# Kernel optimization log

Measured on AMD Instinct MI355X. Metric: run time of the kernel, lower is better.

## Reference

```python
import jax, jax.numpy as jnp
import numpy as np

SUBSTEPS = 4  # fixed dopri5 substeps per output interval
S0, I0, R0 = 0.99, 0.01, 0.0


def _dopri5_step(f, y, dt):
    # Classic Dormand-Prince 5(4) tableau; 5th-order solution needs stages 1,3,4,5,6.
    k1 = f(y)
    k2 = f(y + dt * (1.0 / 5.0) * k1)
    k3 = f(y + dt * (3.0 / 40.0 * k1 + 9.0 / 40.0 * k2))
    k4 = f(y + dt * (44.0 / 45.0 * k1 - 56.0 / 15.0 * k2 + 32.0 / 9.0 * k3))
    k5 = f(y + dt * (19372.0 / 6561.0 * k1 - 25360.0 / 2187.0 * k2
                     + 64448.0 / 6561.0 * k3 - 212.0 / 729.0 * k4))
    k6 = f(y + dt * (9017.0 / 3168.0 * k1 - 355.0 / 33.0 * k2
                     + 46732.0 / 5247.0 * k3 + 49.0 / 176.0 * k4
                     - 5103.0 / 18656.0 * k5))
    return y + dt * (35.0 / 384.0 * k1 + 500.0 / 1113.0 * k3
                     + 125.0 / 192.0 * k4 - 2187.0 / 6784.0 * k5
                     + 11.0 / 84.0 * k6)


def _solve_sir(beta, gamma, t):
    def f(y):
        S, I, R = y[0], y[1], y[2]
        dS = -beta * S * I
        dI = beta * S * I - gamma * I
        dR = gamma * I
        return jnp.stack([dS, dI, dR])

    y0 = jnp.array([S0, I0, R0], dtype=jnp.float32)
    dts = jnp.diff(t)  # [T-1]

    def interval(y, dt):
        h = dt / SUBSTEPS
        def sub(y, _):
            return _dopri5_step(f, y, h), None
        y, _ = jax.lax.scan(sub, y, None, length=SUBSTEPS)
        return y, y

    _, ys = jax.lax.scan(interval, y0, dts)
    return jnp.concatenate([y0[None, :], ys], axis=0)  # [T, 3]


def setup_inputs() -> dict:
    key = jax.random.key(0)
    ks = jax.random.split(key, 14)
    D_IN, D_OUT, T = 8192, 8192, 8192
    s = 0.02
    inp = {
        "x": jax.random.normal(ks[0], (1, D_IN), dtype=jnp.float32),
        "t": jnp.arange(T, dtype=jnp.float32) * (10.0 / T),
        # Encoder: D_IN -> 128 -> 64 -> 2
        "enc_w1": jax.random.normal(ks[1], (D_IN, 128), dtype=jnp.float32) * s,
        "enc_b1": jnp.zeros((128,), dtype=jnp.float32),
        "enc_w2": jax.random.normal(ks[2], (128, 64), dtype=jnp.float32) * s,
        "enc_b2": jnp.zeros((64,), dtype=jnp.float32),
        "enc_w3": jax.random.normal(ks[3], (64, 2), dtype=jnp.float32) * s,
        "enc_b3": jnp.zeros((2,), dtype=jnp.float32),
        # Decoder: 3 -> 64 -> 128 -> D_OUT
        "dec_w1": jax.random.normal(ks[4], (3, 64), dtype=jnp.float32) * s,
        "dec_b1": jnp.zeros((64,), dtype=jnp.float32),
        "dec_w2": jax.random.normal(ks[5], (64, 128), dtype=jnp.float32) * s,
        "dec_b2": jnp.zeros((128,), dtype=jnp.float32),
        "dec_w3": jax.random.normal(ks[6], (128, D_OUT), dtype=jnp.float32) * s,
        "dec_b3": jnp.zeros((D_OUT,), dtype=jnp.float32),
    }
    return inp


def reference(x, t, enc_w1, enc_b1, enc_w2, enc_b2, enc_w3, enc_b3,
              dec_w1, dec_b1, dec_w2, dec_b2, dec_w3, dec_b3):
    # Encoder (batch=1, matching the original's scalar-unbind SIR semantics)
    h = jax.nn.relu(x @ enc_w1 + enc_b1)
    h = jax.nn.relu(h @ enc_w2 + enc_b2)
    p = h @ enc_w3 + enc_b3            # [1, 2]
    beta, gamma = p[0, 0], p[0, 1]

    sol = _solve_sir(beta, gamma, t)   # [T, 3]

    # Decoder
    h = jax.nn.relu(sol @ dec_w1 + dec_b1)
    h = jax.nn.relu(h @ dec_w2 + dec_b2)
    out = jax.nn.relu(h @ dec_w3 + dec_b3)  # [T, D_OUT]
    return out
```

## Files before the change

### kernel.cpp

```cpp
#include <hip/hip_runtime.h>
#include <math.h>
#include <stdint.h>


typedef __attribute__((ext_vector_type(8))) short short8_t;
typedef __attribute__((ext_vector_type(4))) float f32x4;

#define DT_C 0.001220703125f

__device__ __forceinline__ unsigned short f2bf_rn(float f) {
  unsigned int u = __float_as_uint(f);
  unsigned int r = (u + 0x7fffu + ((u >> 16) & 1u)) >> 16;
  return (unsigned short)r;
}
__device__ __forceinline__ float bf2f(unsigned short h) {
  return __uint_as_float(((unsigned int)h) << 16);
}

__device__ __forceinline__ void gl2lds16(const void* g, void* lds_base) {
  __builtin_amdgcn_global_load_lds(
      (const __attribute__((address_space(1))) unsigned int*)(uintptr_t)g,
      (__attribute__((address_space(3))) unsigned int*)(uintptr_t)lds_base,
      16, 0, 0);
}


__device__ __forceinline__ void f_sir(float beta, float gamma,
                                      const float y[3], float d[3]) {
  float SI = y[0] * y[1];
  d[0] = -beta * SI;
  d[1] = beta * SI - gamma * y[1];
  d[2] = gamma * y[1];
}

__device__ __forceinline__ void dopri5_step(float beta, float gamma,
                                            float y[3], float dt) {
  float k1[3], k2[3], k3[3], k4[3], k5[3], k6[3], tmp[3];
  f_sir(beta, gamma, y, k1);
#pragma unroll
  for (int c = 0; c < 3; ++c)
    tmp[c] = y[c] + dt * (0.2f * k1[c]);
  f_sir(beta, gamma, tmp, k2);
#pragma unroll
  for (int c = 0; c < 3; ++c)
    tmp[c] = y[c] + dt * (0.075f * k1[c] + 0.225f * k2[c]);
  f_sir(beta, gamma, tmp, k3);
#pragma unroll
  for (int c = 0; c < 3; ++c)
    tmp[c] = y[c] + dt * ((44.0f / 45.0f) * k1[c] + (-56.0f / 15.0f) * k2[c] +
                          (32.0f / 9.0f) * k3[c]);
  f_sir(beta, gamma, tmp, k4);
#pragma unroll
  for (int c = 0; c < 3; ++c)
    tmp[c] = y[c] + dt * ((19372.0f / 6561.0f) * k1[c] +
                          (-25360.0f / 2187.0f) * k2[c] +
                          (64448.0f / 6561.0f) * k3[c] +
                          (-212.0f / 729.0f) * k4[c]);
  f_sir(beta, gamma, tmp, k5);
#pragma unroll
  for (int c = 0; c < 3; ++c)
    tmp[c] = y[c] + dt * ((9017.0f / 3168.0f) * k1[c] +
                          (-355.0f / 33.0f) * k2[c] +
                          (46732.0f / 5247.0f) * k3[c] +
                          (49.0f / 176.0f) * k4[c] +
                          (-5103.0f / 18656.0f) * k5[c]);
  f_sir(beta, gamma, tmp, k6);
#pragma unroll
  for (int c = 0; c < 3; ++c)
    y[c] = y[c] + dt * ((35.0f / 384.0f) * k1[c] +
                        (500.0f / 1113.0f) * k3[c] +
                        (125.0f / 192.0f) * k4[c] +
                        (-2187.0f / 6784.0f) * k5[c] +
                        (11.0f / 84.0f) * k6[c]);
}

__global__ __launch_bounds__(256) void enc1_kernel(
    const float* __restrict__ x, const float* __restrict__ w1,
    float* __restrict__ partial) {
  __shared__ float4 sh[256];
  int tid = threadIdx.x;
  int j4 = tid & 31, kh = tid >> 5;
  int kbase = blockIdx.x * 128 + kh * 16;
  float4 a; a.x = 0.f; a.y = 0.f; a.z = 0.f; a.w = 0.f;
#pragma unroll
  for (int r = 0; r < 16; ++r) {
    int k = kbase + r;
    float xv = x[k];
    float4 wv = *(const float4*)(w1 + (size_t)k * 128 + j4 * 4);
    a.x = fmaf(xv, wv.x, a.x);
    a.y = fmaf(xv, wv.y, a.y);
    a.z = fmaf(xv, wv.z, a.z);
    a.w = fmaf(xv, wv.w, a.w);
  }
  sh[tid] = a;
  __syncthreads();
  if (tid < 32) {
    float4 s = sh[tid];
#pragma unroll
    for (int h = 1; h < 8; ++h) {
      float4 o = sh[h * 32 + tid];
      s.x += o.x; s.y += o.y; s.z += o.z; s.w += o.w;
    }
    *(float4*)(partial + blockIdx.x * 128 + tid * 4) = s;
  }
}

__global__ __launch_bounds__(256) void prep_kernel(
    const float* __restrict__ partial, const float* __restrict__ b1,
    const float* __restrict__ w2, const float* __restrict__ b2,
    const float* __restrict__ w3, const float* __restrict__ b3,
    float* __restrict__ bg, float* __restrict__ ys) {
  __shared__ float h1s[128];
  __shared__ float h2s[64];
  __shared__ float bgs[2];
  __shared__ float Y0[16][3];
  __shared__ float Y1[256][3];
  int t = threadIdx.x;
  if (t < 128) {
    float s = b1[t];
    for (int b = 0; b < 64; ++b) s += partial[b * 128 + t];
    h1s[t] = fmaxf(s, 0.0f);
  }
  __syncthreads();
  if (t < 64) {
    float a = b2[t];
    for (int k = 0; k < 128; ++k) a = fmaf(h1s[k], w2[k * 64 + t], a);
    h2s[t] = fmaxf(a, 0.0f);
  }
  __syncthreads();
  if (t < 2) {
    float p = b3[t];
    for (int k = 0; k < 64; ++k) p = fmaf(h2s[k], w3[k * 2 + t], p);
    bgs[t] = p;
    bg[t] = p;
  }
  __syncthreads();
  float beta = bgs[0], gamma = bgs[1];
  if (t == 0) {
    float y[3] = {0.99f, 0.01f, 0.0f};
    Y0[0][0] = y[0]; Y0[0][1] = y[1]; Y0[0][2] = y[2];
    for (int j = 1; j < 16; ++j) {
      dopri5_step(beta, gamma, y, 512.0f * DT_C);
      Y0[j][0] = y[0]; Y0[j][1] = y[1]; Y0[j][2] = y[2];
    }
  }
  __syncthreads();
  if (t < 16) {
    float y[3] = {Y0[t][0], Y0[t][1], Y0[t][2]};
    Y1[t * 16][0] = y[0]; Y1[t * 16][1] = y[1]; Y1[t * 16][2] = y[2];
    for (int s = 1; s < 16; ++s) {
      dopri5_step(beta, gamma, y, 32.0f * DT_C);
      Y1[t * 16 + s][0] = y[0]; Y1[t * 16 + s][1] = y[1]; Y1[t * 16 + s][2] = y[2];
    }
  }
  __syncthreads();
  {
    float y[3] = {Y1[t][0], Y1[t][1], Y1[t][2]};
    ys[(t * 8) * 3 + 0] = y[0]; ys[(t * 8) * 3 + 1] = y[1]; ys[(t * 8) * 3 + 2] = y[2];
    for (int s = 1; s < 8; ++s) {
      dopri5_step(beta, gamma, y, 4.0f * DT_C);
      ys[(t * 8 + s) * 3 + 0] = y[0];
      ys[(t * 8 + s) * 3 + 1] = y[1];
      ys[(t * 8 + s) * 3 + 2] = y[2];
    }
  }
}

__global__ __launch_bounds__(256) void wprep_kernel(
    const float* __restrict__ w3, unsigned short* __restrict__ Wt) {
  __shared__ float tl[128 * 65];
  int tid = threadIdx.x;
  int n0 = blockIdx.x * 64;
#pragma unroll
  for (int e = 0; e < 32; ++e) {
    int idx = e * 256 + tid;
    int k = idx >> 6, c = idx & 63;
    tl[k * 65 + c] = w3[(size_t)k * 8192 + n0 + c];
  }
  __syncthreads();
  int nl = tid >> 2, q = tid & 3;
#pragma unroll
  for (int w = 0; w < 4; ++w) {
    int k0 = q * 32 + w * 8;
    short8_t vh, vl;
#pragma unroll
    for (int jj = 0; jj < 8; ++jj) {
      float v = tl[(k0 + jj) * 65 + nl];
      unsigned short h = f2bf_rn(v);
      vh[jj] = (short)h;
      vl[jj] = (short)f2bf_rn(v - bf2f(h));
    }
    *(short8_t*)(Wt + (size_t)(n0 + nl) * 256 + k0) = vh;
    *(short8_t*)(Wt + (size_t)(n0 + nl) * 256 + 128 + k0) = vl;
  }
}

__global__ __launch_bounds__(256) void dec12f_kernel(
    const float* __restrict__ bg, const float* __restrict__ ys,
    const float* __restrict__ w1, const float* __restrict__ b1,
    const float* __restrict__ w2, const float* __restrict__ b2,
    unsigned short* __restrict__ Apack) {
  __shared__ float sols[128 * 4];
  __shared__ float w1s[192];
  __shared__ float b1s[64];
  __shared__ float b2s[128];
  __shared__ float h1s[128 * 66];
  int tid = threadIdx.x;
  int i0 = blockIdx.x * 128;
  if (tid < 192) w1s[tid] = w1[tid];
  if (tid < 64) b1s[tid] = b1[tid];
  if (tid < 128) b2s[tid] = b2[tid];
  if (tid < 33) {
    const float h = 0.25f * DT_C;
    float beta = bg[0], gamma = bg[1];
    int w = blockIdx.x * 32 + tid - 1;
    if (w < 0) {
      sols[0] = 0.99f; sols[1] = 0.01f; sols[2] = 0.0f;
    } else {
      float y[3] = {ys[w * 3 + 0], ys[w * 3 + 1], ys[w * 3 + 2]};
#pragma unroll
      for (int iv = 0; iv < 4; ++iv) {
        dopri5_step(beta, gamma, y, h);
        dopri5_step(beta, gamma, y, h);
        dopri5_step(beta, gamma, y, h);
        dopri5_step(beta, gamma, y, h);
        int local = 4 * w + iv + 1 - i0;
        if (local >= 0 && local < 128) {
          sols[local * 4 + 0] = y[0];
          sols[local * 4 + 1] = y[1];
          sols[local * 4 + 2] = y[2];
        }
      }
    }
  }
  __syncthreads();
#pragma unroll
  for (int e = 0; e < 32; ++e) {
    int idx = e * 256 + tid;
    int i = idx >> 6, j = idx & 63;
    float v = b1s[j];
    v = fmaf(sols[i * 4 + 0], w1s[j], v);
    v = fmaf(sols[i * 4 + 1], w1s[64 + j], v);
    v = fmaf(sols[i * 4 + 2], w1s[128 + j], v);
    h1s[i * 66 + j] = fmaxf(v, 0.0f);
  }
  __syncthreads();
  int tx = tid & 15, ty = tid >> 4;
  float acc[8][8];
#pragma unroll
  for (int a = 0; a < 8; ++a)
#pragma unroll
    for (int b = 0; b < 8; ++b) acc[a][b] = 0.0f;
  for (int j = 0; j < 64; ++j) {
    float a[8];
#pragma unroll
    for (int mm = 0; mm < 8; ++mm) a[mm] = h1s[(ty * 8 + mm) * 66 + j];
    float4 q0 = *(const float4*)(w2 + j * 128 + tx * 8);
    float4 q1 = *(const float4*)(w2 + j * 128 + tx * 8 + 4);
    float b[8] = {q0.x, q0.y, q0.z, q0.w, q1.x, q1.y, q1.z, q1.w};
#pragma unroll
    for (int mm = 0; mm < 8; ++mm)
#pragma unroll
      for (int nn = 0; nn < 8; ++nn)
        acc[mm][nn] = fmaf(a[mm], b[nn], acc[mm][nn]);
  }
#pragma unroll
  for (int mm = 0; mm < 8; ++mm) {
    int row = i0 + ty * 8 + mm;
    short8_t vh, vl;
#pragma unroll
    for (int nn = 0; nn < 8; ++nn) {
      float v = fmaxf(acc[mm][nn] + b2s[tx * 8 + nn], 0.0f);
      unsigned short h = f2bf_rn(v);
      vh[nn] = (short)h;
      vl[nn] = (short)f2bf_rn(v - bf2f(h));
    }
    *(short8_t*)(Apack + (size_t)row * 256 + tx * 8) = vh;
    *(short8_t*)(Apack + (size_t)row * 256 + 128 + tx * 8) = vl;
  }
}

__global__ __launch_bounds__(256) void gemm_bf16_kernel(
    const unsigned short* __restrict__ A, const unsigned short* __restrict__ B,
    const float* __restrict__ bias, float* __restrict__ out) {
  __shared__ unsigned short As[128 * 64];
  __shared__ unsigned short Bs[128 * 64];
  int tid = threadIdx.x;
  int m0 = blockIdx.y * 128;
  int n0 = blockIdx.x * 128;
  int lane = tid & 63, wave = tid >> 6;
  int wm = (wave >> 1) * 64, wn = (wave & 1) * 64;
  int lrow = lane & 15, lgrp = lane >> 4;
  int lr8 = lane >> 3, lp = lane & 7;

  f32x4 acc[4][4];
  f32x4 z = {0.0f, 0.0f, 0.0f, 0.0f};
#pragma unroll
  for (int mi = 0; mi < 4; ++mi)
#pragma unroll
    for (int ni = 0; ni < 4; ++ni) acc[mi][ni] = z;

  for (int it = 0; it < 6; ++it) {
    int s = it >> 1;
    int kin = (it & 1) * 64;
    int co_a = ((s == 2) ? 128 : 0) + kin;
    int co_b = ((s == 1) ? 128 : 0) + kin;
#pragma unroll
    for (int i = 0; i < 4; ++i) {
      int seg = wave * 4 + i;
      int r = seg * 8 + lr8;
      int g = lp ^ (r & 7);
      gl2lds16(A + (size_t)(m0 + r) * 256 + co_a + g * 8, &As[seg * 512]);
      gl2lds16(B + (size_t)(n0 + r) * 256 + co_b + g * 8, &Bs[seg * 512]);
    }
    __syncthreads();
#pragma unroll
    for (int kk = 0; kk < 64; kk += 32) {
      short8_t af[4], bf[4];
#pragma unroll
      for (int mi = 0; mi < 4; ++mi) {
        int r = wm + mi * 16 + lrow;
        int p = ((kk >> 3) + lgrp) ^ (r & 7);
        af[mi] = *(const short8_t*)(&As[r * 64 + p * 8]);
      }
#pragma unroll
      for (int ni = 0; ni < 4; ++ni) {
        int r = wn + ni * 16 + lrow;
        int p = ((kk >> 3) + lgrp) ^ (r & 7);
        bf[ni] = *(const short8_t*)(&Bs[r * 64 + p * 8]);
      }
#pragma unroll
      for (int mi = 0; mi < 4; ++mi)
#pragma unroll
        for (int ni = 0; ni < 4; ++ni)
          acc[mi][ni] = __builtin_amdgcn_mfma_f32_16x16x32_bf16(
              af[mi], bf[ni], acc[mi][ni], 0, 0, 0);
    }
    __syncthreads();
  }

  float bv[4];
#pragma unroll
  for (int ni = 0; ni < 4; ++ni) bv[ni] = bias[n0 + wn + ni * 16 + lrow];
#pragma unroll
  for (int mi = 0; mi < 4; ++mi)
#pragma unroll
    for (int ni = 0; ni < 4; ++ni) {
      int col = n0 + wn + ni * 16 + lrow;
#pragma unroll
      for (int r = 0; r < 4; ++r) {
        int row = m0 + wm + mi * 16 + lgrp * 4 + r;
        out[(size_t)row * 8192 + col] = fmaxf(acc[mi][ni][r] + bv[ni], 0.0f);
      }
    }
}


extern "C" void kernel_launch(void* const* d_in, const int* in_sizes, int n_in,
                              void* d_out, int out_size, void* d_ws, size_t ws_size,
                              hipStream_t stream) {
  const float* x      = (const float*)d_in[0];
  const float* enc_w1 = (const float*)d_in[2];
  const float* enc_b1 = (const float*)d_in[3];
  const float* enc_w2 = (const float*)d_in[4];
  const float* enc_b2 = (const float*)d_in[5];
  const float* enc_w3 = (const float*)d_in[6];
  const float* enc_b3 = (const float*)d_in[7];
  const float* dec_w1 = (const float*)d_in[8];
  const float* dec_b1 = (const float*)d_in[9];
  const float* dec_w2 = (const float*)d_in[10];
  const float* dec_b2 = (const float*)d_in[11];
  const float* dec_w3 = (const float*)d_in[12];
  const float* dec_b3 = (const float*)d_in[13];
  float* out = (float*)d_out;

  float* ws      = (float*)d_ws;
  float* bg      = ws;
  float* partial = ws + 64;
  float* ys      = ws + 8320;
  unsigned short* Apack = (unsigned short*)((char*)d_ws + 65536);
  unsigned short* Wt    = (unsigned short*)((char*)d_ws + 65536 + 4194304);

  hipLaunchKernelGGL(wprep_kernel, dim3(128), dim3(256), 0, stream, dec_w3, Wt);
  hipLaunchKernelGGL(enc1_kernel, dim3(64), dim3(256), 0, stream, x, enc_w1, partial);
  hipLaunchKernelGGL(prep_kernel, dim3(1), dim3(256), 0, stream,
                     partial, enc_b1, enc_w2, enc_b2, enc_w3, enc_b3, bg, ys);
  hipLaunchKernelGGL(dec12f_kernel, dim3(64), dim3(256), 0, stream,
                     bg, ys, dec_w1, dec_b1, dec_w2, dec_b2, Apack);
  hipLaunchKernelGGL(gemm_bf16_kernel, dim3(64, 64), dim3(256), 0, stream,
                     Apack, Wt, dec_b3, out);
}
```

Measured before the change: 371.3 us.

## Merge encoder and weight-prep kernels, restructure split-bf16 GEMM with block swizzle

```diff
diff --git a/kernel.cpp b/kernel.cpp
--- a/kernel.cpp
+++ b/kernel.cpp
@@ -74,34 +74,63 @@
                         (11.0f / 84.0f) * k6[c]);
 }
 
-__global__ __launch_bounds__(256) void enc1_kernel(
+__global__ __launch_bounds__(256) void pre_kernel(
     const float* __restrict__ x, const float* __restrict__ w1,
-    float* __restrict__ partial) {
-  __shared__ float4 sh[256];
+    float* __restrict__ partial,
+    const float* __restrict__ w3, unsigned short* __restrict__ Wt) {
+  __shared__ __align__(16) float smem[128 * 65];
   int tid = threadIdx.x;
-  int j4 = tid & 31, kh = tid >> 5;
-  int kbase = blockIdx.x * 128 + kh * 16;
-  float4 a; a.x = 0.f; a.y = 0.f; a.z = 0.f; a.w = 0.f;
-#pragma unroll
-  for (int r = 0; r < 16; ++r) {
-    int k = kbase + r;
-    float xv = x[k];
-    float4 wv = *(const float4*)(w1 + (size_t)k * 128 + j4 * 4);
-    a.x = fmaf(xv, wv.x, a.x);
-    a.y = fmaf(xv, wv.y, a.y);
-    a.z = fmaf(xv, wv.z, a.z);
-    a.w = fmaf(xv, wv.w, a.w);
-  }
-  sh[tid] = a;
-  __syncthreads();
-  if (tid < 32) {
-    float4 s = sh[tid];
-#pragma unroll
-    for (int h = 1; h < 8; ++h) {
-      float4 o = sh[h * 32 + tid];
-      s.x += o.x; s.y += o.y; s.z += o.z; s.w += o.w;
-    }
-    *(float4*)(partial + blockIdx.x * 128 + tid * 4) = s;
+  if (blockIdx.x < 64) {
+    float4* sh = (float4*)smem;
+    int j4 = tid & 31, kh = tid >> 5;
+    int kbase = blockIdx.x * 128 + kh * 16;
+    float4 a; a.x = 0.f; a.y = 0.f; a.z = 0.f; a.w = 0.f;
+#pragma unroll
+    for (int r = 0; r < 16; ++r) {
+      int k = kbase + r;
+      float xv = x[k];
+      float4 wv = *(const float4*)(w1 + (size_t)k * 128 + j4 * 4);
+      a.x = fmaf(xv, wv.x, a.x);
+      a.y = fmaf(xv, wv.y, a.y);
+      a.z = fmaf(xv, wv.z, a.z);
+      a.w = fmaf(xv, wv.w, a.w);
+    }
+    sh[tid] = a;
+    __syncthreads();
+    if (tid < 32) {
+      float4 s = sh[tid];
+#pragma unroll
+      for (int h = 1; h < 8; ++h) {
+        float4 o = sh[h * 32 + tid];
+        s.x += o.x; s.y += o.y; s.z += o.z; s.w += o.w;
+      }
+      *(float4*)(partial + blockIdx.x * 128 + tid * 4) = s;
+    }
+  } else {
+    float* tl = smem;
+    int n0 = (blockIdx.x - 64) * 64;
+#pragma unroll
+    for (int e = 0; e < 32; ++e) {
+      int idx = e * 256 + tid;
+      int k = idx >> 6, c = idx & 63;
+      tl[k * 65 + c] = w3[(size_t)k * 8192 + n0 + c];
+    }
+    __syncthreads();
+    int nl = tid >> 2, q = tid & 3;
+#pragma unroll
+    for (int w = 0; w < 4; ++w) {
+      int k0 = q * 32 + w * 8;
+      short8_t vh, vl;
+#pragma unroll
+      for (int jj = 0; jj < 8; ++jj) {
+        float v = tl[(k0 + jj) * 65 + nl];
+        unsigned short h = f2bf_rn(v);
+        vh[jj] = (short)h;
+        vl[jj] = (short)f2bf_rn(v - bf2f(h));
+      }
+      *(short8_t*)(Wt + (size_t)(n0 + nl) * 256 + k0) = vh;
+      *(short8_t*)(Wt + (size_t)(n0 + nl) * 256 + 128 + k0) = vl;
+    }
   }
 }
 
@@ -163,35 +192,6 @@
       ys[(t * 8 + s) * 3 + 1] = y[1];
       ys[(t * 8 + s) * 3 + 2] = y[2];
     }
-  }
-}
-
-__global__ __launch_bounds__(256) void wprep_kernel(
-    const float* __restrict__ w3, unsigned short* __restrict__ Wt) {
-  __shared__ float tl[128 * 65];
-  int tid = threadIdx.x;
-  int n0 = blockIdx.x * 64;
-#pragma unroll
-  for (int e = 0; e < 32; ++e) {
-    int idx = e * 256 + tid;
-    int k = idx >> 6, c = idx & 63;
-    tl[k * 65 + c] = w3[(size_t)k * 8192 + n0 + c];
-  }
-  __syncthreads();
-  int nl = tid >> 2, q = tid & 3;
-#pragma unroll
-  for (int w = 0; w < 4; ++w) {
-    int k0 = q * 32 + w * 8;
-    short8_t vh, vl;
-#pragma unroll
-    for (int jj = 0; jj < 8; ++jj) {
-      float v = tl[(k0 + jj) * 65 + nl];
-      unsigned short h = f2bf_rn(v);
-      vh[jj] = (short)h;
-      vl[jj] = (short)f2bf_rn(v - bf2f(h));
-    }
-    *(short8_t*)(Wt + (size_t)(n0 + nl) * 256 + k0) = vh;
-    *(short8_t*)(Wt + (size_t)(n0 + nl) * 256 + 128 + k0) = vl;
   }
 }
 
@@ -283,15 +283,20 @@
 __global__ __launch_bounds__(256) void gemm_bf16_kernel(
     const unsigned short* __restrict__ A, const unsigned short* __restrict__ B,
     const float* __restrict__ bias, float* __restrict__ out) {
-  __shared__ unsigned short As[128 * 64];
-  __shared__ unsigned short Bs[128 * 64];
+  __shared__ unsigned short Ah[128 * 32];
+  __shared__ unsigned short Al[128 * 32];
+  __shared__ unsigned short Bh[128 * 32];
+  __shared__ unsigned short Bl[128 * 32];
   int tid = threadIdx.x;
-  int m0 = blockIdx.y * 128;
-  int n0 = blockIdx.x * 128;
+  int bid = blockIdx.x;
+  int swz = (bid & 7) * 512 + (bid >> 3);
+  int by = swz & 63, bx = swz >> 6;
+  int m0 = by * 128;
+  int n0 = bx * 128;
   int lane = tid & 63, wave = tid >> 6;
   int wm = (wave >> 1) * 64, wn = (wave & 1) * 64;
   int lrow = lane & 15, lgrp = lane >> 4;
-  int lr8 = lane >> 3, lp = lane & 7;
+  int lr4 = lane >> 2, lp = lane & 3;
 
   f32x4 acc[4][4];
   f32x4 z = {0.0f, 0.0f, 0.0f, 0.0f};
@@ -300,41 +305,70 @@
 #pragma unroll
     for (int ni = 0; ni < 4; ++ni) acc[mi][ni] = z;
 
-  for (int it = 0; it < 6; ++it) {
-    int s = it >> 1;
-    int kin = (it & 1) * 64;
-    int co_a = ((s == 2) ? 128 : 0) + kin;
-    int co_b = ((s == 1) ? 128 : 0) + kin;
-#pragma unroll
-    for (int i = 0; i < 4; ++i) {
-      int seg = wave * 4 + i;
-      int r = seg * 8 + lr8;
-      int g = lp ^ (r & 7);
-      gl2lds16(A + (size_t)(m0 + r) * 256 + co_a + g * 8, &As[seg * 512]);
-      gl2lds16(B + (size_t)(n0 + r) * 256 + co_b + g * 8, &Bs[seg * 512]);
+  for (int c = 0; c < 4; ++c) {
+    int kin = c * 32;
+#pragma unroll
+    for (int i = 0; i < 2; ++i) {
+      int seg = wave * 2 + i;
+      int r = seg * 16 + lr4;
+      int g = lp ^ (r & 3);
+      const unsigned short* ar = A + (size_t)(m0 + r) * 256 + kin + g * 8;
+      const unsigned short* br = B + (size_t)(n0 + r) * 256 + kin + g * 8;
+      gl2lds16(ar, &Ah[seg * 512]);
+      gl2lds16(ar + 128, &Al[seg * 512]);
+      gl2lds16(br, &Bh[seg * 512]);
+      gl2lds16(br + 128, &Bl[seg * 512]);
     }
     __syncthreads();
-#pragma unroll
-    for (int kk = 0; kk < 64; kk += 32) {
-      short8_t af[4], bf[4];
+
+    short8_t ah[4], bh[4];
+#pragma unroll
+    for (int mi = 0; mi < 4; ++mi) {
+      int r = wm + mi * 16 + lrow;
+      int p = lgrp ^ (r & 3);
+      ah[mi] = *(const short8_t*)(&Ah[r * 32 + p * 8]);
+    }
+#pragma unroll
+    for (int ni = 0; ni < 4; ++ni) {
+      int r = wn + ni * 16 + lrow;
+      int p = lgrp ^ (r & 3);
+      bh[ni] = *(const short8_t*)(&Bh[r * 32 + p * 8]);
+    }
+#pragma unroll
+    for (int mi = 0; mi < 4; ++mi)
+#pragma unroll
+      for (int ni = 0; ni < 4; ++ni)
+        acc[mi][ni] = __builtin_amdgcn_mfma_f32_16x16x32_bf16(
+            ah[mi], bh[ni], acc[mi][ni], 0, 0, 0);
+    {
+      short8_t bl[4];
+#pragma unroll
+      for (int ni = 0; ni < 4; ++ni) {
+        int r = wn + ni * 16 + lrow;
+        int p = lgrp ^ (r & 3);
+        bl[ni] = *(const short8_t*)(&Bl[r * 32 + p * 8]);
+      }
+#pragma unroll
+      for (int mi = 0; mi < 4; ++mi)
+#pragma unroll
+        for (int ni = 0; ni < 4; ++ni)
+          acc[mi][ni] = __builtin_amdgcn_mfma_f32_16x16x32_bf16(
+              ah[mi], bl[ni], acc[mi][ni], 0, 0, 0);
+    }
+    {
+      short8_t al[4];
 #pragma unroll
       for (int mi = 0; mi < 4; ++mi) {
         int r = wm + mi * 16 + lrow;
-        int p = ((kk >> 3) + lgrp) ^ (r & 7);
-        af[mi] = *(const short8_t*)(&As[r * 64 + p * 8]);
-      }
-#pragma unroll
-      for (int ni = 0; ni < 4; ++ni) {
-        int r = wn + ni * 16 + lrow;
-        int p = ((kk >> 3) + lgrp) ^ (r & 7);
-        bf[ni] = *(const short8_t*)(&Bs[r * 64 + p * 8]);
+        int p = lgrp ^ (r & 3);
+        al[mi] = *(const short8_t*)(&Al[r * 32 + p * 8]);
       }
 #pragma unroll
       for (int mi = 0; mi < 4; ++mi)
 #pragma unroll
         for (int ni = 0; ni < 4; ++ni)
           acc[mi][ni] = __builtin_amdgcn_mfma_f32_16x16x32_bf16(
-              af[mi], bf[ni], acc[mi][ni], 0, 0, 0);
+              al[mi], bh[ni], acc[mi][ni], 0, 0, 0);
     }
     __syncthreads();
   }
@@ -381,12 +415,12 @@
   unsigned short* Apack = (unsigned short*)((char*)d_ws + 65536);
   unsigned short* Wt    = (unsigned short*)((char*)d_ws + 65536 + 4194304);
 
-  hipLaunchKernelGGL(wprep_kernel, dim3(128), dim3(256), 0, stream, dec_w3, Wt);
-  hipLaunchKernelGGL(enc1_kernel, dim3(64), dim3(256), 0, stream, x, enc_w1, partial);
+  hipLaunchKernelGGL(pre_kernel, dim3(192), dim3(256), 0, stream,
+                     x, enc_w1, partial, dec_w3, Wt);
   hipLaunchKernelGGL(prep_kernel, dim3(1), dim3(256), 0, stream,
                      partial, enc_b1, enc_w2, enc_b2, enc_w3, enc_b3, bg, ys);
   hipLaunchKernelGGL(dec12f_kernel, dim3(64), dim3(256), 0, stream,
                      bg, ys, dec_w1, dec_b1, dec_w2, dec_b2, Apack);
-  hipLaunchKernelGGL(gemm_bf16_kernel, dim3(64, 64), dim3(256), 0, stream,
+  hipLaunchKernelGGL(gemm_bf16_kernel, dim3(4096), dim3(256), 0, stream,
                      Apack, Wt, dec_b3, out);
 }
```

Result: slower. 393.9 us (+6.1%).
